# Optimization experiments

Hardware: AMD Instinct MI355X
Metric: run time of the kernel (lower is better)

## Reference

```python
import jax, jax.numpy as jnp
import numpy as np

BN_EPS = 1e-5

def _group(x, idx):
    # x: [B, N, C], idx: [B, N, K] -> [B, N, K, C]
    return jax.vmap(lambda a, i: a[i])(x, idx)

def _mlp_bn_relu(h, W, b, g, beta):
    # 1x1 Conv2d == per-point channel matmul; BN in training mode (batch stats)
    h = jnp.einsum('bnkc,oc->bnko', h, W) + b
    mu = h.mean(axis=(0, 1, 2))
    var = h.var(axis=(0, 1, 2))  # biased, matches torch BN normalization
    h = (h - mu) * jax.lax.rsqrt(var + BN_EPS) * g + beta
    return jax.nn.relu(h)

def setup_inputs() -> dict:
    key = jax.random.key(0)
    ks = jax.random.split(key, 8)
    B, N, D = 8, 4096, 64
    inp = {
        'xyz': jax.random.normal(ks[0], (B, N, 3), jnp.float32),
        'points': jax.random.normal(ks[1], (B, N, D), jnp.float32),
        'W0': jax.random.normal(ks[2], (64, 67), jnp.float32) * 0.1,
        'b0': jnp.zeros((64,), jnp.float32),
        'g0': jnp.ones((64,), jnp.float32),
        'beta0': jnp.zeros((64,), jnp.float32),
        'W1': jax.random.normal(ks[3], (64, 64), jnp.float32) * 0.1,
        'b1': jnp.zeros((64,), jnp.float32),
        'g1': jnp.ones((64,), jnp.float32),
        'beta1': jnp.zeros((64,), jnp.float32),
        'W2': jax.random.normal(ks[4], (128, 64), jnp.float32) * 0.1,
        'b2': jnp.zeros((128,), jnp.float32),
        'g2': jnp.ones((128,), jnp.float32),
        'beta2': jnp.zeros((128,), jnp.float32),
        'nsample': 32,
    }
    return inp

def reference(xyz, points, W0, b0, g0, beta0, W1, b1, g1, beta1, W2, b2, g2, beta2, nsample):
    B, N, C = xyz.shape
    sq = jnp.sum(xyz * xyz, axis=-1)
    dists = sq[:, :, None] + sq[:, None, :] - 2.0 * jnp.einsum('bnc,bmc->bnm', xyz, xyz)
    # k smallest distances (original uses full argsort; same selected set)
    _, idx = jax.lax.top_k(-dists, nsample)  # [B, N, K]
    grouped_xyz_norm = _group(xyz, idx) - xyz[:, :, None, :]   # [B, N, K, 3]
    grouped_points = _group(points, idx)                        # [B, N, K, D]
    h = jnp.concatenate([grouped_xyz_norm, grouped_points], axis=-1)  # [B, N, K, 3+D]
    for W, b, g, beta in ((W0, b0, g0, beta0), (W1, b1, g1, beta1), (W2, b2, g2, beta2)):
        h = _mlp_bn_relu(h, W, b, g, beta)
    return jnp.max(h, axis=2)  # max over neighbors -> [B, N, C_out]
```

## Files before the change

kernel.cpp:

```cpp
#include <hip/hip_runtime.h>


using half4  = __attribute__((ext_vector_type(4))) _Float16;
using half8  = __attribute__((ext_vector_type(8))) _Float16;
using floatx4 = __attribute__((ext_vector_type(4))) float;

#define NB 8
#define NP 4096
#define NQ (NB*NP)
#define CNT_INV (1.0f/1048576.0f)

#define OFF_XYZ4  0ull
#define OFF_Q     (OFF_XYZ4 + (size_t)NQ*4*4)
#define OFF_R     (OFF_Q    + (size_t)NQ*64*4)
#define OFF_IDX   (OFF_R    + (size_t)NQ*64*4)
#define OFF_W1H   (OFF_IDX  + (size_t)NQ*32*4)
#define OFF_W2H   (OFF_W1H  + 4096*2)
#define OFF_P0    (OFF_W2H  + 8192*2)
#define OFF_P1    (OFF_P0   + (size_t)1024*128*4)
#define OFF_P2    (OFF_P1   + (size_t)1024*128*4)
#define OFF_PAR   (OFF_P2   + (size_t)1024*256*4)
#define OFF_MMAX  (OFF_PAR  + 512*4)
#define OFF_MMIN  (OFF_MMAX + (size_t)NQ*128*4)
#define OFF_P0BIG OFF_MMAX
#define OFF_Q0    OFF_P0
#define OFF_Q1    (OFF_P0 + (size_t)64*128*4)
#define OFF_Q2    (OFF_P0 + (size_t)2*64*128*4)

__global__ __launch_bounds__(256) void k_prep(
    const float* __restrict__ xyz, const float* __restrict__ points,
    const float* __restrict__ W0, const float* __restrict__ b0,
    const float* __restrict__ W1, const float* __restrict__ W2,
    float* __restrict__ xyz4, float* __restrict__ Q, float* __restrict__ R,
    _Float16* __restrict__ W1h, _Float16* __restrict__ W2h) {
  if (blockIdx.x >= NQ/4) {
    int t = (blockIdx.x - NQ/4)*256 + threadIdx.x;
    if (t < 4096) W1h[t] = (_Float16)W1[t];
    if (t < 8192) W2h[t] = (_Float16)W2[t];
    return;
  }
  __shared__ float w0s[64*67];
  for (int i = threadIdx.x; i < 64*67; i += 256) w0s[i] = W0[i];
  __syncthreads();
  int p = blockIdx.x*4 + (threadIdx.x >> 6);
  int o = threadIdx.x & 63;
  float x = xyz[p*3+0], y = xyz[p*3+1], z = xyz[p*3+2];
  const float* wr = w0s + o*67;
  float q = wr[0]*x + wr[1]*y + wr[2]*z;
  float r = b0[o] + q;
  const float4* pp4 = (const float4*)(points + (size_t)p*64);
  #pragma unroll
  for (int c4 = 0; c4 < 16; ++c4) {
    float4 pv = pp4[c4];
    r = fmaf(wr[3+4*c4+0], pv.x, r);
    r = fmaf(wr[3+4*c4+1], pv.y, r);
    r = fmaf(wr[3+4*c4+2], pv.z, r);
    r = fmaf(wr[3+4*c4+3], pv.w, r);
  }
  Q[(size_t)p*64 + o] = q;
  R[(size_t)p*64 + o] = r;
  if (o == 0) {
    float sq = fmaf(x,x, fmaf(y,y, z*z));
    xyz4[p*4+0]=x; xyz4[p*4+1]=y; xyz4[p*4+2]=z; xyz4[p*4+3]=sq;
  }
}

__device__ __forceinline__ unsigned fmap(float f) {
  unsigned u = __float_as_uint(f);
  return u ^ ((unsigned)((int)u >> 31) | 0x80000000u);
}

#define INSERT_ROUND(uu, jj)                                                  \
  {                                                                           \
    unsigned long long ball = __ballot((uu) <= utau && (uu) < thr);           \
    while (ball) {                                                            \
      int src = __ffsll(ball) - 1;                                            \
      ball &= ball - 1;                                                       \
      unsigned cu = (unsigned)__builtin_amdgcn_readlane((int)(uu), src);      \
      int cj = __builtin_amdgcn_readlane((jj), src);                          \
      if (cu < thr) {                                                         \
        unsigned long long m = __ballot(lane < 32 && ku < cu);                \
        int pos = __popcll(m);                                                \
        unsigned ku_up = __shfl_up(ku, 1);                                    \
        int jv_up = __shfl_up(jv, 1);                                         \
        if (lane < 32) {                                                      \
          if (lane > pos)      { ku = ku_up; jv = jv_up; }                    \
          else if (lane == pos){ ku = cu;    jv = cj;    }                    \
        }                                                                     \
        thr = (unsigned)__builtin_amdgcn_readlane((int)ku, 31);               \
      }                                                                       \
    }                                                                         \
  }

__global__ __launch_bounds__(256, 6) void k_knn(
    const float* __restrict__ xyz4, int* __restrict__ idxb,
    const float* __restrict__ R, const float* __restrict__ Q,
    float* __restrict__ p0) {
  const int lane = threadIdx.x & 63;
  const int w = threadIdx.x >> 6;
  const int qid = blockIdx.x * 4 + w;
  const int b = qid >> 12;
  const float4* xb = (const float4*)xyz4 + (size_t)b * NP;
  const float4 qv = xb[qid & (NP-1)];
  int* op = idxb + (size_t)qid * 32;

  float mn = __uint_as_float(0x7F800000u);
  {
    float mn1 = mn, mn2 = mn, mn3 = mn;
    #pragma unroll 4
    for (int c = 32; c < 64; c += 4) {
      float4 a0 = xb[(c+0)*64 + lane];
      float4 a1 = xb[(c+1)*64 + lane];
      float4 a2 = xb[(c+2)*64 + lane];
      float4 a3 = xb[(c+3)*64 + lane];
      float d0 = fmaf(-2.0f, fmaf(qv.x,a0.x, fmaf(qv.y,a0.y, qv.z*a0.z)), qv.w + a0.w);
      float d1 = fmaf(-2.0f, fmaf(qv.x,a1.x, fmaf(qv.y,a1.y, qv.z*a1.z)), qv.w + a1.w);
      float d2 = fmaf(-2.0f, fmaf(qv.x,a2.x, fmaf(qv.y,a2.y, qv.z*a2.z)), qv.w + a2.w);
      float d3 = fmaf(-2.0f, fmaf(qv.x,a3.x, fmaf(qv.y,a3.y, qv.z*a3.z)), qv.w + a3.w);
      mn = fminf(mn, d0); mn1 = fminf(mn1, d1);
      mn2 = fminf(mn2, d2); mn3 = fminf(mn3, d3);
    }
    mn = fminf(fminf(mn, mn1), fminf(mn2, mn3));
  }

  float dvA[32];
  #pragma unroll
  for (int c = 0; c < 32; ++c) {
    float4 cd = xb[c*64 + lane];
    float dot = fmaf(qv.x, cd.x, fmaf(qv.y, cd.y, qv.z*cd.z));
    float d   = fmaf(-2.0f, dot, qv.w + cd.w);
    dvA[c] = d;
    mn = fminf(mn, d);
  }

  const unsigned mu = fmap(mn);
  unsigned lo = 0u, hi = 0xFFFFFFFFu;
  for (int it = 0; it < 32; ++it) {
    unsigned mid = lo + ((hi - lo) >> 1);
    int cnt = __popcll(__ballot(mu <= mid));
    if (cnt >= 32) hi = mid; else lo = mid + 1;
  }
  const unsigned utau = hi;

  unsigned ku = 0xFFFFFFFFu;
  int jv = 0;
  unsigned thr = 0xFFFFFFFFu;
  #pragma unroll
  for (int c = 0; c < 32; ++c) {
    unsigned u = fmap(dvA[c]);
    int j = c*64 + lane;
    INSERT_ROUND(u, j)
  }
  #pragma unroll 8
  for (int c = 32; c < 64; ++c) {
    float4 cd = xb[c*64 + lane];
    float dot = fmaf(qv.x, cd.x, fmaf(qv.y, cd.y, qv.z*cd.z));
    float d   = fmaf(-2.0f, dot, qv.w + cd.w);
    unsigned u = fmap(d);
    int j = c*64 + lane;
    INSERT_ROUND(u, j)
  }
  if (lane < 32) op[lane] = jv;

  const float* Rb2 = R + (size_t)(qid & ~(NP-1))*64;
  const float  qc  = Q[(size_t)qid*64 + lane];
  float s = 0.f, ss = 0.f;
  #pragma unroll 8
  for (int k = 0; k < 32; ++k) {
    int j = __shfl(jv, k);
    float v = Rb2[(size_t)j*64 + lane] - qc;
    s += v; ss = fmaf(v, v, ss);
  }
  __shared__ float red[4][128];
  red[w][lane]      = s;
  red[w][64 + lane] = ss;
  __syncthreads();
  if (w == 0) {
    float S  = red[0][lane]    + red[1][lane]    + red[2][lane]    + red[3][lane];
    float SS = red[0][64+lane] + red[1][64+lane] + red[2][64+lane] + red[3][64+lane];
    p0[(size_t)blockIdx.x*128 + lane]      = S;
    p0[(size_t)blockIdx.x*128 + 64 + lane] = SS;
  }
}

template<int W, int RPB>
__global__ __launch_bounds__(256) void k_redg(
    const float* __restrict__ pin, float* __restrict__ pout) {
  constexpr int G   = 256 / W;
  constexpr int RPG = RPB / G;
  int r   = blockIdx.x;
  int col = threadIdx.x % W;
  int g   = threadIdx.x / W;
  const float* base = pin + ((size_t)r*RPB + (size_t)g*RPG)*W + col;
  float s = 0.f;
  #pragma unroll
  for (int i = 0; i < RPG; ++i) s += base[(size_t)i*W];
  if constexpr (G == 1) {
    pout[(size_t)r*W + col] = s;
  } else {
    __shared__ float rr[G][W];
    rr[g][col] = s;
    __syncthreads();
    if (threadIdx.x < W) {
      float t = rr[0][threadIdx.x];
      #pragma unroll
      for (int gg = 1; gg < G; ++gg) t += rr[gg][threadIdx.x];
      pout[(size_t)r*W + threadIdx.x] = t;
    }
  }
}

template<int NPARTS>
__global__ void k_fin(const float* __restrict__ part, int C,
                      const float* __restrict__ g, const float* __restrict__ beta,
                      float* __restrict__ par, int poff) {
  int o = threadIdx.x;
  float S = 0.f, SS = 0.f;
  #pragma unroll
  for (int s = 0; s < NPARTS; ++s) {
    S  += part[s*2*C + o];
    SS += part[s*2*C + C + o];
  }
  float mu  = S * CNT_INV;
  float var = SS * CNT_INV - mu*mu;
  float sc  = g[o] * rsqrtf(var + 1e-5f);
  par[poff + o]     = sc;
  par[poff + C + o] = beta[o] - mu*sc;
}

#define BUILD_X1(q0)                                                          \
  {                                                                           \
    int qid = (q0) + aql;                                                     \
    const float* Rb = R + (size_t)(qid & ~4095)*64;                           \
    const int* ix = idxb + (size_t)qid*32;                                    \
    float4 Q4 = ((const float4*)(Q + (size_t)qid*64))[aseg];                  \
    float qx = fmaf(-Q4.x, asc.x, ash.x);                                     \
    float qy = fmaf(-Q4.y, asc.y, ash.y);                                     \
    float qz = fmaf(-Q4.z, asc.z, ash.z);                                     \
    float qw = fmaf(-Q4.w, asc.w, ash.w);                                     \
    _Pragma("unroll")                                                         \
    for (int i = 0; i < 8; ++i) {                                             \
      int k = arg + (i<<2);                                                   \
      int j = ix[k];                                                          \
      float4 R4 = ((const float4*)(Rb + (size_t)j*64))[aseg];                 \
      float v0 = fmaxf(fmaf(R4.x, asc.x, qx), 0.f);                           \
      float v1 = fmaxf(fmaf(R4.y, asc.y, qy), 0.f);                           \
      float v2 = fmaxf(fmaf(R4.z, asc.z, qz), 0.f);                           \
      float v3 = fmaxf(fmaf(R4.w, asc.w, qw), 0.f);                           \
      half4 hv = {(_Float16)v0, (_Float16)v1, (_Float16)v2, (_Float16)v3};    \
      *(half4*)(x1 + (aql*32 + k)*72 + aseg*4) = hv;                          \
    }                                                                         \
  }

__global__ __launch_bounds__(256) void k_l1(
    const float* __restrict__ R, const float* __restrict__ Q,
    const int* __restrict__ idxb, const _Float16* __restrict__ W1h,
    const float* __restrict__ b1, const float* __restrict__ par,
    float* __restrict__ p1) {
  __shared__ __align__(16) _Float16 x1[128*72];
  int o = threadIdx.x & 63, wg = threadIdx.x >> 6;
  int m16 = o & 15, quad = o >> 4;
  const int aql = threadIdx.x >> 6;
  const int arg = (threadIdx.x >> 4) & 3;
  const int aseg = threadIdx.x & 15;
  const float4 asc = ((const float4*)par)[aseg];
  const float4 ash = ((const float4*)(par+64))[aseg];
  int col = wg*16 + m16;
  half8 bf0 = *(const half8*)(W1h + col*64 + quad*8);
  half8 bf1 = *(const half8*)(W1h + col*64 + 32 + quad*8);
  float b1c = b1[col];
  float s = 0.f, ss = 0.f;

  for (int gi = 0; gi < 8; ++gi) {
    int q0 = (blockIdx.x*8 + gi) * 4;
    BUILD_X1(q0)
    __syncthreads();
    #pragma unroll
    for (int rt = 0; rt < 8; ++rt) {
      const _Float16* ap = x1 + (rt*16 + m16)*72 + quad*8;
      half8 a0 = *(const half8*)(ap);
      half8 a1 = *(const half8*)(ap + 32);
      floatx4 acc = {0.f,0.f,0.f,0.f};
      acc = __builtin_amdgcn_mfma_f32_16x16x32_f16(a0, bf0, acc, 0,0,0);
      acc = __builtin_amdgcn_mfma_f32_16x16x32_f16(a1, bf1, acc, 0,0,0);
      #pragma unroll
      for (int rg = 0; rg < 4; ++rg) {
        float h = acc[rg] + b1c;
        s += h; ss = fmaf(h, h, ss);
      }
    }
    __syncthreads();
  }
  s  += __shfl_xor(s, 16);  s  += __shfl_xor(s, 32);
  ss += __shfl_xor(ss, 16); ss += __shfl_xor(ss, 32);
  if (quad == 0) {
    p1[blockIdx.x*128 + col]      = s;
    p1[blockIdx.x*128 + 64 + col] = ss;
  }
}

__global__ __launch_bounds__(256) void k_l2(
    const float* __restrict__ R, const float* __restrict__ Q,
    const int* __restrict__ idxb, const _Float16* __restrict__ W1h,
    const _Float16* __restrict__ W2h, const float* __restrict__ b1,
    const float* __restrict__ b2, const float* __restrict__ par,
    float* __restrict__ p2, float* __restrict__ Mmax, float* __restrict__ Mmin) {
  __shared__ __align__(16) _Float16 x1[128*72];
  __shared__ __align__(16) _Float16 x2[128*72];
  int o = threadIdx.x & 63, wg = threadIdx.x >> 6;
  int m16 = o & 15, quad = o >> 4;
  const int aql = threadIdx.x >> 6;
  const int arg = (threadIdx.x >> 4) & 3;
  const int aseg = threadIdx.x & 15;
  const float4 asc = ((const float4*)par)[aseg];
  const float4 ash = ((const float4*)(par+64))[aseg];
  int col1 = wg*16 + m16;
  float sc1 = par[128 + col1], sh1 = par[192 + col1];
  half8 b1f0 = *(const half8*)(W1h + col1*64 + quad*8);
  half8 b1f1 = *(const half8*)(W1h + col1*64 + 32 + quad*8);
  float b1c = b1[col1];
  int colA = wg*16 + m16, colB = 64 + wg*16 + m16;
  half8 b2A0 = *(const half8*)(W2h + colA*64 + quad*8);
  half8 b2A1 = *(const half8*)(W2h + colA*64 + 32 + quad*8);
  half8 b2B0 = *(const half8*)(W2h + colB*64 + quad*8);
  half8 b2B1 = *(const half8*)(W2h + colB*64 + 32 + quad*8);
  float b2a = b2[colA], b2b = b2[colB];
  float sA=0.f, ssA=0.f, sB=0.f, ssB=0.f;

  for (int gi = 0; gi < 8; ++gi) {
    int q0 = (blockIdx.x*8 + gi) * 4;
    BUILD_X1(q0)
    __syncthreads();
    #pragma unroll
    for (int rt = 0; rt < 8; ++rt) {
      const _Float16* ap = x1 + (rt*16 + m16)*72 + quad*8;
      half8 a0 = *(const half8*)(ap);
      half8 a1 = *(const half8*)(ap + 32);
      floatx4 acc = {0.f,0.f,0.f,0.f};
      acc = __builtin_amdgcn_mfma_f32_16x16x32_f16(a0, b1f0, acc, 0,0,0);
      acc = __builtin_amdgcn_mfma_f32_16x16x32_f16(a1, b1f1, acc, 0,0,0);
      #pragma unroll
      for (int rg = 0; rg < 4; ++rg) {
        float h = acc[rg] + b1c;
        float v = fmaxf(fmaf(h, sc1, sh1), 0.f);
        x2[(rt*16 + quad*4 + rg)*72 + col1] = (_Float16)v;
      }
    }
    __syncthreads();
    float mxA=0.f, mnA=0.f, mxB=0.f, mnB=0.f;
    #pragma unroll
    for (int rt = 0; rt < 8; ++rt) {
      const _Float16* ap = x2 + (rt*16 + m16)*72 + quad*8;
      half8 a0 = *(const half8*)(ap);
      half8 a1 = *(const half8*)(ap + 32);
      floatx4 accA = {0.f,0.f,0.f,0.f}, accB = {0.f,0.f,0.f,0.f};
      accA = __builtin_amdgcn_mfma_f32_16x16x32_f16(a0, b2A0, accA, 0,0,0);
      accA = __builtin_amdgcn_mfma_f32_16x16x32_f16(a1, b2A1, accA, 0,0,0);
      accB = __builtin_amdgcn_mfma_f32_16x16x32_f16(a0, b2B0, accB, 0,0,0);
      accB = __builtin_amdgcn_mfma_f32_16x16x32_f16(a1, b2B1, accB, 0,0,0);
      float hA0 = accA[0]+b2a, hA1 = accA[1]+b2a, hA2 = accA[2]+b2a, hA3 = accA[3]+b2a;
      float hB0 = accB[0]+b2b, hB1 = accB[1]+b2b, hB2 = accB[2]+b2b, hB3 = accB[3]+b2b;
      sA += hA0+hA1+hA2+hA3;
      ssA = fmaf(hA0,hA0, fmaf(hA1,hA1, fmaf(hA2,hA2, fmaf(hA3,hA3, ssA))));
      sB += hB0+hB1+hB2+hB3;
      ssB = fmaf(hB0,hB0, fmaf(hB1,hB1, fmaf(hB2,hB2, fmaf(hB3,hB3, ssB))));
      float m4A = fmaxf(fmaxf(hA0,hA1), fmaxf(hA2,hA3));
      float n4A = fminf(fminf(hA0,hA1), fminf(hA2,hA3));
      float m4B = fmaxf(fmaxf(hB0,hB1), fmaxf(hB2,hB3));
      float n4B = fminf(fminf(hB0,hB1), fminf(hB2,hB3));
      if ((rt & 1) == 0) { mxA=m4A; mnA=n4A; mxB=m4B; mnB=n4B; }
      else {
        mxA=fmaxf(mxA,m4A); mnA=fminf(mnA,n4A);
        mxB=fmaxf(mxB,m4B); mnB=fminf(mnB,n4B);
        mxA=fmaxf(mxA,__shfl_xor(mxA,16)); mxA=fmaxf(mxA,__shfl_xor(mxA,32));
        mnA=fminf(mnA,__shfl_xor(mnA,16)); mnA=fminf(mnA,__shfl_xor(mnA,32));
        mxB=fmaxf(mxB,__shfl_xor(mxB,16)); mxB=fmaxf(mxB,__shfl_xor(mxB,32));
        mnB=fminf(mnB,__shfl_xor(mnB,16)); mnB=fminf(mnB,__shfl_xor(mnB,32));
        if (quad == 0) {
          int qid = q0 + (rt >> 1);
          Mmax[(size_t)qid*128 + colA] = mxA;  Mmin[(size_t)qid*128 + colA] = mnA;
          Mmax[(size_t)qid*128 + colB] = mxB;  Mmin[(size_t)qid*128 + colB] = mnB;
        }
      }
    }
    __syncthreads();
  }
  sA += __shfl_xor(sA,16); sA += __shfl_xor(sA,32);
  ssA += __shfl_xor(ssA,16); ssA += __shfl_xor(ssA,32);
  sB += __shfl_xor(sB,16); sB += __shfl_xor(sB,32);
  ssB += __shfl_xor(ssB,16); ssB += __shfl_xor(ssB,32);
  if (quad == 0) {
    p2[blockIdx.x*256 + colA]        = sA;
    p2[blockIdx.x*256 + 128 + colA]  = ssA;
    p2[blockIdx.x*256 + colB]        = sB;
    p2[blockIdx.x*256 + 128 + colB]  = ssB;
  }
}

__global__ __launch_bounds__(256) void k_out(
    const float* __restrict__ Mmax, const float* __restrict__ Mmin,
    const float* __restrict__ par, float* __restrict__ out) {
  int t = blockIdx.x*256 + threadIdx.x;
  int seg = t & 31;
  float4 sc = ((const float4*)(par+256))[seg];
  float4 sh = ((const float4*)(par+384))[seg];
  float4 mx = ((const float4*)Mmax)[t];
  float4 mn = ((const float4*)Mmin)[t];
  float4 o;
  o.x = fmaxf(fmaf(sc.x >= 0.f ? mx.x : mn.x, sc.x, sh.x), 0.f);
  o.y = fmaxf(fmaf(sc.y >= 0.f ? mx.y : mn.y, sc.y, sh.y), 0.f);
  o.z = fmaxf(fmaf(sc.z >= 0.f ? mx.z : mn.z, sc.z, sh.z), 0.f);
  o.w = fmaxf(fmaf(sc.w >= 0.f ? mx.w : mn.w, sc.w, sh.w), 0.f);
  ((float4*)out)[t] = o;
}

extern "C" void kernel_launch(void* const* d_in, const int* in_sizes, int n_in,
                              void* d_out, int out_size, void* d_ws, size_t ws_size,
                              hipStream_t stream) {
  const float* xyz    = (const float*)d_in[0];
  const float* points = (const float*)d_in[1];
  const float* W0     = (const float*)d_in[2];
  const float* b0     = (const float*)d_in[3];
  const float* g0     = (const float*)d_in[4];
  const float* beta0  = (const float*)d_in[5];
  const float* W1     = (const float*)d_in[6];
  const float* b1     = (const float*)d_in[7];
  const float* g1     = (const float*)d_in[8];
  const float* beta1  = (const float*)d_in[9];
  const float* W2     = (const float*)d_in[10];
  const float* b2     = (const float*)d_in[11];
  const float* g2     = (const float*)d_in[12];
  const float* beta2  = (const float*)d_in[13];

  char* ws = (char*)d_ws;
  float*     xyz4 = (float*)(ws + OFF_XYZ4);
  float*     Qb   = (float*)(ws + OFF_Q);
  float*     Rb   = (float*)(ws + OFF_R);
  int*       idxb = (int*)  (ws + OFF_IDX);
  _Float16*  W1h  = (_Float16*)(ws + OFF_W1H);
  _Float16*  W2h  = (_Float16*)(ws + OFF_W2H);
  float*     q0   = (float*)(ws + OFF_Q0);
  float*     q1   = (float*)(ws + OFF_Q1);
  float*     q2   = (float*)(ws + OFF_Q2);
  float*     p0b  = (float*)(ws + OFF_P0BIG);
  float*     p1   = (float*)(ws + OFF_P1);
  float*     p2   = (float*)(ws + OFF_P2);
  float*     par  = (float*)(ws + OFF_PAR);
  float*     Mmax = (float*)(ws + OFF_MMAX);
  float*     Mmin = (float*)(ws + OFF_MMIN);
  float*     out  = (float*)d_out;

  hipLaunchKernelGGL(k_prep,  dim3(NQ/4 + 32), dim3(256), 0, stream,
                     xyz, points, W0, b0, W1, W2, xyz4, Qb, Rb, W1h, W2h);
  hipLaunchKernelGGL(k_knn,   dim3(NQ/4), dim3(256), 0, stream, xyz4, idxb, Rb, Qb, p0b);
  hipLaunchKernelGGL((k_redg<128,128>), dim3(64), dim3(256), 0, stream, p0b, q0);
  hipLaunchKernelGGL((k_fin<64>),   dim3(1), dim3(64),  0, stream, q0, 64, g0, beta0, par, 0);
  hipLaunchKernelGGL(k_l1,    dim3(1024), dim3(256), 0, stream, Rb, Qb, idxb, W1h, b1, par, p1);
  hipLaunchKernelGGL((k_redg<128,16>),  dim3(64), dim3(256), 0, stream, p1, q1);
  hipLaunchKernelGGL((k_fin<64>),   dim3(1), dim3(64),  0, stream, q1, 64, g1, beta1, par, 128);
  hipLaunchKernelGGL(k_l2,    dim3(1024), dim3(256), 0, stream, Rb, Qb, idxb, W1h, W2h, b1, b2, par, p2, Mmax, Mmin);
  hipLaunchKernelGGL((k_redg<256,16>),  dim3(64), dim3(256), 0, stream, p2, q2);
  hipLaunchKernelGGL((k_fin<64>),   dim3(1), dim3(128), 0, stream, q2, 128, g2, beta2, par, 256);
  hipLaunchKernelGGL(k_out,   dim3(out_size/1024), dim3(256), 0, stream, Mmax, Mmin, par, out);
}
```

Baseline: 398.4 us.

## Materialize layer-1 pre-BN activations in fp16 and skip recompute in layer 2

When the workspace is large enough, layer 1 stores its pre-BN fp16 activations to a global buffer, and a new layer-2 kernel reads them back instead of regathering neighbours and redoing the first MFMA layer. This trades the gather and layer-1 recomputation for writing and reading about 128 MB of fp16 activations. The prep kernel also handles 16 points per block instead of 4. The old path is kept as a fallback when the workspace is too small.

```diff
diff --git a/kernel.cpp b/kernel.cpp
--- a/kernel.cpp
+++ b/kernel.cpp
@@ -22,6 +22,8 @@
 #define OFF_PAR   (OFF_P2   + (size_t)1024*256*4)
 #define OFF_MMAX  (OFF_PAR  + 512*4)
 #define OFF_MMIN  (OFF_MMAX + (size_t)NQ*128*4)
+#define OFF_H1    (OFF_MMIN + (size_t)NQ*128*4)
+#define WS_NEED   (OFF_H1   + (size_t)NQ*32*64*2)
 #define OFF_P0BIG OFF_MMAX
 #define OFF_Q0    OFF_P0
 #define OFF_Q1    (OFF_P0 + (size_t)64*128*4)
@@ -33,8 +35,8 @@
     const float* __restrict__ W1, const float* __restrict__ W2,
     float* __restrict__ xyz4, float* __restrict__ Q, float* __restrict__ R,
     _Float16* __restrict__ W1h, _Float16* __restrict__ W2h) {
-  if (blockIdx.x >= NQ/4) {
-    int t = (blockIdx.x - NQ/4)*256 + threadIdx.x;
+  if (blockIdx.x >= NQ/16) {
+    int t = (blockIdx.x - NQ/16)*256 + threadIdx.x;
     if (t < 4096) W1h[t] = (_Float16)W1[t];
     if (t < 8192) W2h[t] = (_Float16)W2[t];
     return;
@@ -42,26 +44,29 @@
   __shared__ float w0s[64*67];
   for (int i = threadIdx.x; i < 64*67; i += 256) w0s[i] = W0[i];
   __syncthreads();
-  int p = blockIdx.x*4 + (threadIdx.x >> 6);
   int o = threadIdx.x & 63;
-  float x = xyz[p*3+0], y = xyz[p*3+1], z = xyz[p*3+2];
   const float* wr = w0s + o*67;
-  float q = wr[0]*x + wr[1]*y + wr[2]*z;
-  float r = b0[o] + q;
-  const float4* pp4 = (const float4*)(points + (size_t)p*64);
   #pragma unroll
-  for (int c4 = 0; c4 < 16; ++c4) {
-    float4 pv = pp4[c4];
-    r = fmaf(wr[3+4*c4+0], pv.x, r);
-    r = fmaf(wr[3+4*c4+1], pv.y, r);
-    r = fmaf(wr[3+4*c4+2], pv.z, r);
-    r = fmaf(wr[3+4*c4+3], pv.w, r);
-  }
-  Q[(size_t)p*64 + o] = q;
-  R[(size_t)p*64 + o] = r;
-  if (o == 0) {
-    float sq = fmaf(x,x, fmaf(y,y, z*z));
-    xyz4[p*4+0]=x; xyz4[p*4+1]=y; xyz4[p*4+2]=z; xyz4[p*4+3]=sq;
+  for (int pl = 0; pl < 4; ++pl) {
+    int p = blockIdx.x*16 + pl*4 + (threadIdx.x >> 6);
+    float x = xyz[p*3+0], y = xyz[p*3+1], z = xyz[p*3+2];
+    float q = wr[0]*x + wr[1]*y + wr[2]*z;
+    float r = b0[o] + q;
+    const float4* pp4 = (const float4*)(points + (size_t)p*64);
+    #pragma unroll
+    for (int c4 = 0; c4 < 16; ++c4) {
+      float4 pv = pp4[c4];
+      r = fmaf(wr[3+4*c4+0], pv.x, r);
+      r = fmaf(wr[3+4*c4+1], pv.y, r);
+      r = fmaf(wr[3+4*c4+2], pv.z, r);
+      r = fmaf(wr[3+4*c4+3], pv.w, r);
+    }
+    Q[(size_t)p*64 + o] = q;
+    R[(size_t)p*64 + o] = r;
+    if (o == 0) {
+      float sq = fmaf(x,x, fmaf(y,y, z*z));
+      xyz4[p*4+0]=x; xyz4[p*4+1]=y; xyz4[p*4+2]=z; xyz4[p*4+3]=sq;
+    }
   }
 }
 
@@ -252,12 +257,14 @@
     }                                                                         \
   }
 
+template<bool STORE>
 __global__ __launch_bounds__(256) void k_l1(
     const float* __restrict__ R, const float* __restrict__ Q,
     const int* __restrict__ idxb, const _Float16* __restrict__ W1h,
     const float* __restrict__ b1, const float* __restrict__ par,
-    float* __restrict__ p1) {
+    float* __restrict__ p1, _Float16* __restrict__ h1p) {
   __shared__ __align__(16) _Float16 x1[128*72];
+  __shared__ __align__(16) _Float16 x2s[STORE ? 128*72 : 8];
   int o = threadIdx.x & 63, wg = threadIdx.x >> 6;
   int m16 = o & 15, quad = o >> 4;
   const int aql = threadIdx.x >> 6;
@@ -287,9 +294,18 @@
       for (int rg = 0; rg < 4; ++rg) {
         float h = acc[rg] + b1c;
         s += h; ss = fmaf(h, h, ss);
+        if constexpr (STORE)
+          x2s[(rt*16 + quad*4 + rg)*72 + col] = (_Float16)h;
       }
     }
     __syncthreads();
+    if constexpr (STORE) {
+      int row = threadIdx.x >> 1, hs = threadIdx.x & 1;
+      const float4* srcp = (const float4*)(x2s + (size_t)row*72 + hs*32);
+      float4* dstp = (float4*)(h1p + ((size_t)q0*32 + (size_t)row)*64 + hs*32);
+      #pragma unroll
+      for (int i = 0; i < 4; ++i) dstp[i] = srcp[i];
+    }
   }
   s  += __shfl_xor(s, 16);  s  += __shfl_xor(s, 32);
   ss += __shfl_xor(ss, 16); ss += __shfl_xor(ss, 32);
@@ -299,26 +315,19 @@
   }
 }
 
-__global__ __launch_bounds__(256) void k_l2(
-    const float* __restrict__ R, const float* __restrict__ Q,
-    const int* __restrict__ idxb, const _Float16* __restrict__ W1h,
-    const _Float16* __restrict__ W2h, const float* __restrict__ b1,
+__global__ __launch_bounds__(256) void k_l2f(
+    const _Float16* __restrict__ h1p, const _Float16* __restrict__ W2h,
     const float* __restrict__ b2, const float* __restrict__ par,
     float* __restrict__ p2, float* __restrict__ Mmax, float* __restrict__ Mmin) {
-  __shared__ __align__(16) _Float16 x1[128*72];
   __shared__ __align__(16) _Float16 x2[128*72];
   int o = threadIdx.x & 63, wg = threadIdx.x >> 6;
   int m16 = o & 15, quad = o >> 4;
-  const int aql = threadIdx.x >> 6;
-  const int arg = (threadIdx.x >> 4) & 3;
-  const int aseg = threadIdx.x & 15;
-  const float4 asc = ((const float4*)par)[aseg];
-  const float4 ash = ((const float4*)(par+64))[aseg];
-  int col1 = wg*16 + m16;
-  float sc1 = par[128 + col1], sh1 = par[192 + col1];
-  half8 b1f0 = *(const half8*)(W1h + col1*64 + quad*8);
-  half8 b1f1 = *(const half8*)(W1h + col1*64 + 32 + quad*8);
-  float b1c = b1[col1];
+  const int c8 = (threadIdx.x & 7) * 8;
+  const int rb = threadIdx.x >> 3;
+  const float4 sc1a = *(const float4*)(par + 128 + c8);
+  const float4 sc1b = *(const float4*)(par + 128 + c8 + 4);
+  const float4 sh1a = *(const float4*)(par + 192 + c8);
+  const float4 sh1b = *(const float4*)(par + 192 + c8 + 4);
   int colA = wg*16 + m16, colB = 64 + wg*16 + m16;
   half8 b2A0 = *(const half8*)(W2h + colA*64 + quad*8);
   half8 b2A1 = *(const half8*)(W2h + colA*64 + 32 + quad*8);
@@ -329,22 +338,21 @@
 
   for (int gi = 0; gi < 8; ++gi) {
     int q0 = (blockIdx.x*8 + gi) * 4;
-    BUILD_X1(q0)
-    __syncthreads();
+    const _Float16* gsrc = h1p + (size_t)q0*2048;
     #pragma unroll
-    for (int rt = 0; rt < 8; ++rt) {
-      const _Float16* ap = x1 + (rt*16 + m16)*72 + quad*8;
-      half8 a0 = *(const half8*)(ap);
-      half8 a1 = *(const half8*)(ap + 32);
-      floatx4 acc = {0.f,0.f,0.f,0.f};
-      acc = __builtin_amdgcn_mfma_f32_16x16x32_f16(a0, b1f0, acc, 0,0,0);
-      acc = __builtin_amdgcn_mfma_f32_16x16x32_f16(a1, b1f1, acc, 0,0,0);
-      #pragma unroll
-      for (int rg = 0; rg < 4; ++rg) {
-        float h = acc[rg] + b1c;
-        float v = fmaxf(fmaf(h, sc1, sh1), 0.f);
-        x2[(rt*16 + quad*4 + rg)*72 + col1] = (_Float16)v;
-      }
+    for (int i = 0; i < 4; ++i) {
+      int r = rb + 32*i;
+      half8 hv = *(const half8*)(gsrc + (size_t)r*64 + c8);
+      half8 ov;
+      ov[0] = (_Float16)fmaxf(fmaf((float)hv[0], sc1a.x, sh1a.x), 0.f);
+      ov[1] = (_Float16)fmaxf(fmaf((float)hv[1], sc1a.y, sh1a.y), 0.f);
+      ov[2] = (_Float16)fmaxf(fmaf((float)hv[2], sc1a.z, sh1a.z), 0.f);
+      ov[3] = (_Float16)fmaxf(fmaf((float)hv[3], sc1a.w, sh1a.w), 0.f);
+      ov[4] = (_Float16)fmaxf(fmaf((float)hv[4], sc1b.x, sh1b.x), 0.f);
+      ov[5] = (_Float16)fmaxf(fmaf((float)hv[5], sc1b.y, sh1b.y), 0.f);
+      ov[6] = (_Float16)fmaxf(fmaf((float)hv[6], sc1b.z, sh1b.z), 0.f);
+      ov[7] = (_Float16)fmaxf(fmaf((float)hv[7], sc1b.w, sh1b.w), 0.f);
+      *(half8*)(x2 + (size_t)r*72 + c8) = ov;
     }
     __syncthreads();
     float mxA=0.f, mnA=0.f, mxB=0.f, mnB=0.f;
@@ -397,6 +405,104 @@
   }
 }
 
+__global__ __launch_bounds__(256) void k_l2(
+    const float* __restrict__ R, const float* __restrict__ Q,
+    const int* __restrict__ idxb, const _Float16* __restrict__ W1h,
+    const _Float16* __restrict__ W2h, const float* __restrict__ b1,
+    const float* __restrict__ b2, const float* __restrict__ par,
+    float* __restrict__ p2, float* __restrict__ Mmax, float* __restrict__ Mmin) {
+  __shared__ __align__(16) _Float16 x1[128*72];
+  __shared__ __align__(16) _Float16 x2[128*72];
+  int o = threadIdx.x & 63, wg = threadIdx.x >> 6;
+  int m16 = o & 15, quad = o >> 4;
+  const int aql = threadIdx.x >> 6;
+  const int arg = (threadIdx.x >> 4) & 3;
+  const int aseg = threadIdx.x & 15;
+  const float4 asc = ((const float4*)par)[aseg];
+  const float4 ash = ((const float4*)(par+64))[aseg];
+  int col1 = wg*16 + m16;
+  float sc1 = par[128 + col1], sh1 = par[192 + col1];
+  half8 b1f0 = *(const half8*)(W1h + col1*64 + quad*8);
+  half8 b1f1 = *(const half8*)(W1h + col1*64 + 32 + quad*8);
+  float b1c = b1[col1];
+  int colA = wg*16 + m16, colB = 64 + wg*16 + m16;
+  half8 b2A0 = *(const half8*)(W2h + colA*64 + quad*8);
+  half8 b2A1 = *(const half8*)(W2h + colA*64 + 32 + quad*8);
+  half8 b2B0 = *(const half8*)(W2h + colB*64 + quad*8);
+  half8 b2B1 = *(const half8*)(W2h + colB*64 + 32 + quad*8);
+  float b2a = b2[colA], b2b = b2[colB];
+  float sA=0.f, ssA=0.f, sB=0.f, ssB=0.f;
+
+  for (int gi = 0; gi < 8; ++gi) {
+    int q0 = (blockIdx.x*8 + gi) * 4;
+    BUILD_X1(q0)
+    __syncthreads();
+    #pragma unroll
+    for (int rt = 0; rt < 8; ++rt) {
+      const _Float16* ap = x1 + (rt*16 + m16)*72 + quad*8;
+      half8 a0 = *(const half8*)(ap);
+      half8 a1 = *(const half8*)(ap + 32);
+      floatx4 acc = {0.f,0.f,0.f,0.f};
+      acc = __builtin_amdgcn_mfma_f32_16x16x32_f16(a0, b1f0, acc, 0,0,0);
+      acc = __builtin_amdgcn_mfma_f32_16x16x32_f16(a1, b1f1, acc, 0,0,0);
+      #pragma unroll
+      for (int rg = 0; rg < 4; ++rg) {
+        float h = acc[rg] + b1c;
+        float v = fmaxf(fmaf(h, sc1, sh1), 0.f);
+        x2[(rt*16 + quad*4 + rg)*72 + col1] = (_Float16)v;
+      }
+    }
+    __syncthreads();
+    float mxA=0.f, mnA=0.f, mxB=0.f, mnB=0.f;
+    #pragma unroll
+    for (int rt = 0; rt < 8; ++rt) {
+      const _Float16* ap = x2 + (rt*16 + m16)*72 + quad*8;
+      half8 a0 = *(const half8*)(ap);
+      half8 a1 = *(const half8*)(ap + 32);
+      floatx4 accA = {0.f,0.f,0.f,0.f}, accB = {0.f,0.f,0.f,0.f};
+      accA = __builtin_amdgcn_mfma_f32_16x16x32_f16(a0, b2A0, accA, 0,0,0);
+      accA = __builtin_amdgcn_mfma_f32_16x16x32_f16(a1, b2A1, accA, 0,0,0);
+      accB = __builtin_amdgcn_mfma_f32_16x16x32_f16(a0, b2B0, accB, 0,0,0);
+      accB = __builtin_amdgcn_mfma_f32_16x16x32_f16(a1, b2B1, accB, 0,0,0);
+      float hA0 = accA[0]+b2a, hA1 = accA[1]+b2a, hA2 = accA[2]+b2a, hA3 = accA[3]+b2a;
+      float hB0 = accB[0]+b2b, hB1 = accB[1]+b2b, hB2 = accB[2]+b2b, hB3 = accB[3]+b2b;
+      sA += hA0+hA1+hA2+hA3;
+      ssA = fmaf(hA0,hA0, fmaf(hA1,hA1, fmaf(hA2,hA2, fmaf(hA3,hA3, ssA))));
+      sB += hB0+hB1+hB2+hB3;
+      ssB = fmaf(hB0,hB0, fmaf(hB1,hB1, fmaf(hB2,hB2, fmaf(hB3,hB3, ssB))));
+      float m4A = fmaxf(fmaxf(hA0,hA1), fmaxf(hA2,hA3));
+      float n4A = fminf(fminf(hA0,hA1), fminf(hA2,hA3));
+      float m4B = fmaxf(fmaxf(hB0,hB1), fmaxf(hB2,hB3));
+      float n4B = fminf(fminf(hB0,hB1), fminf(hB2,hB3));
+      if ((rt & 1) == 0) { mxA=m4A; mnA=n4A; mxB=m4B; mnB=n4B; }
+      else {
+        mxA=fmaxf(mxA,m4A); mnA=fminf(mnA,n4A);
+        mxB=fmaxf(mxB,m4B); mnB=fminf(mnB,n4B);
+        mxA=fmaxf(mxA,__shfl_xor(mxA,16)); mxA=fmaxf(mxA,__shfl_xor(mxA,32));
+        mnA=fminf(mnA,__shfl_xor(mnA,16)); mnA=fminf(mnA,__shfl_xor(mnA,32));
+        mxB=fmaxf(mxB,__shfl_xor(mxB,16)); mxB=fmaxf(mxB,__shfl_xor(mxB,32));
+        mnB=fminf(mnB,__shfl_xor(mnB,16)); mnB=fminf(mnB,__shfl_xor(mnB,32));
+        if (quad == 0) {
+          int qid = q0 + (rt >> 1);
+          Mmax[(size_t)qid*128 + colA] = mxA;  Mmin[(size_t)qid*128 + colA] = mnA;
+          Mmax[(size_t)qid*128 + colB] = mxB;  Mmin[(size_t)qid*128 + colB] = mnB;
+        }
+      }
+    }
+    __syncthreads();
+  }
+  sA += __shfl_xor(sA,16); sA += __shfl_xor(sA,32);
+  ssA += __shfl_xor(ssA,16); ssA += __shfl_xor(ssA,32);
+  sB += __shfl_xor(sB,16); sB += __shfl_xor(sB,32);
+  ssB += __shfl_xor(ssB,16); ssB += __shfl_xor(ssB,32);
+  if (quad == 0) {
+    p2[blockIdx.x*256 + colA]        = sA;
+    p2[blockIdx.x*256 + 128 + colA]  = ssA;
+    p2[blockIdx.x*256 + colB]        = sB;
+    p2[blockIdx.x*256 + 128 + colB]  = ssB;
+  }
+}
+
 __global__ __launch_bounds__(256) void k_out(
     const float* __restrict__ Mmax, const float* __restrict__ Mmin,
     const float* __restrict__ par, float* __restrict__ out) {
@@ -448,17 +554,32 @@
   float*     par  = (float*)(ws + OFF_PAR);
   float*     Mmax = (float*)(ws + OFF_MMAX);
   float*     Mmin = (float*)(ws + OFF_MMIN);
+  _Float16*  h1p  = (_Float16*)(ws + OFF_H1);
   float*     out  = (float*)d_out;
 
-  hipLaunchKernelGGL(k_prep,  dim3(NQ/4 + 32), dim3(256), 0, stream,
+  const bool big = (ws_size >= WS_NEED);
+
+  hipLaunchKernelGGL(k_prep,  dim3(NQ/16 + 32), dim3(256), 0, stream,
                      xyz, points, W0, b0, W1, W2, xyz4, Qb, Rb, W1h, W2h);
   hipLaunchKernelGGL(k_knn,   dim3(NQ/4), dim3(256), 0, stream, xyz4, idxb, Rb, Qb, p0b);
   hipLaunchKernelGGL((k_redg<128,128>), dim3(64), dim3(256), 0, stream, p0b, q0);
   hipLaunchKernelGGL((k_fin<64>),   dim3(1), dim3(64),  0, stream, q0, 64, g0, beta0, par, 0);
-  hipLaunchKernelGGL(k_l1,    dim3(1024), dim3(256), 0, stream, Rb, Qb, idxb, W1h, b1, par, p1);
+  if (big) {
+    hipLaunchKernelGGL((k_l1<true>),  dim3(1024), dim3(256), 0, stream,
+                       Rb, Qb, idxb, W1h, b1, par, p1, h1p);
+  } else {
+    hipLaunchKernelGGL((k_l1<false>), dim3(1024), dim3(256), 0, stream,
+                       Rb, Qb, idxb, W1h, b1, par, p1, h1p);
+  }
   hipLaunchKernelGGL((k_redg<128,16>),  dim3(64), dim3(256), 0, stream, p1, q1);
   hipLaunchKernelGGL((k_fin<64>),   dim3(1), dim3(64),  0, stream, q1, 64, g1, beta1, par, 128);
-  hipLaunchKernelGGL(k_l2,    dim3(1024), dim3(256), 0, stream, Rb, Qb, idxb, W1h, W2h, b1, b2, par, p2, Mmax, Mmin);
+  if (big) {
+    hipLaunchKernelGGL(k_l2f, dim3(1024), dim3(256), 0, stream,
+                       h1p, W2h, b2, par, p2, Mmax, Mmin);
+  } else {
+    hipLaunchKernelGGL(k_l2,  dim3(1024), dim3(256), 0, stream,
+                       Rb, Qb, idxb, W1h, W2h, b1, b2, par, p2, Mmax, Mmin);
+  }
   hipLaunchKernelGGL((k_redg<256,16>),  dim3(64), dim3(256), 0, stream, p2, q2);
   hipLaunchKernelGGL((k_fin<64>),   dim3(1), dim3(128), 0, stream, q2, 128, g2, beta2, par, 256);
   hipLaunchKernelGGL(k_out,   dim3(out_size/1024), dim3(256), 0, stream, Mmax, Mmin, par, out);
```

Result: slower. 435.4 us (+9.3%).
